# Kernel optimization log

Hardware: AMD Instinct MI355X
Metric: run time of the kernel (lower is better)

## Reference

```python
import jax, jax.numpy as jnp
import numpy as np

NUM_HEAD = 8
HIDDEN = 128
INPUT_DIM = 256
N1 = 1024
N2 = 1024
BATCH = 16


def setup_inputs() -> dict:
    key = jax.random.key(0)
    ks = jax.random.split(key, 10)
    HD = HIDDEN * NUM_HEAD  # 1024
    return {
        "x1": jax.random.normal(ks[0], (BATCH, N1, INPUT_DIM), jnp.float32),
        "x2": jax.random.normal(ks[1], (BATCH, N2, INPUT_DIM), jnp.float32),
        "B": jax.random.normal(ks[2], (N1, N2), jnp.float32),
        "wq_w": jax.random.normal(ks[3], (HD, INPUT_DIM), jnp.float32) * 0.02,
        "wq_b": jnp.zeros((HD,), jnp.float32),
        "wk_w": jax.random.normal(ks[4], (HD, INPUT_DIM), jnp.float32) * 0.02,
        "wk_b": jnp.zeros((HD,), jnp.float32),
        "wv_w": jax.random.normal(ks[5], (HD, INPUT_DIM), jnp.float32) * 0.02,
        "wv_b": jnp.zeros((HD,), jnp.float32),
        "proj_w": jax.random.normal(ks[6], (HIDDEN, HD), jnp.float32) * 0.02,
        "proj_b": jnp.zeros((HIDDEN,), jnp.float32),
    }


def reference(x1, x2, B, wq_w, wq_b, wk_w, wk_b, wv_w, wv_b, proj_w, proj_b):
    b, n1, _ = x1.shape
    n2 = x2.shape[1]
    sdk = jnp.sqrt(jnp.asarray(HIDDEN, x1.dtype))
    # Linear layers (torch convention: y = x @ W.T + b)
    q = x1 @ wq_w.T + wq_b                      # [b, n1, H*D]
    k = x2 @ wk_w.T + wk_b                      # [b, n2, H*D]
    v = x2 @ wv_w.T + wv_b                      # [b, n2, H*D]
    q = q.reshape(b, n1, NUM_HEAD, HIDDEN)
    k = k.reshape(b, n2, NUM_HEAD, HIDDEN)
    v = v.reshape(b, n2, NUM_HEAD, HIDDEN)
    # scores: [b, h, n1, n2]
    scores = jnp.einsum("bnhd,bmhd->bhnm", q, k) / sdk + B[None, None, :, :]
    attn = jax.nn.softmax(scores, axis=-1)
    out = jnp.einsum("bhnm,bmhd->bnhd", attn, v).reshape(b, n1, NUM_HEAD * HIDDEN)
    return out @ proj_w.T + proj_b              # [b, n1, HIDDEN]
```

## Files before the change

### kernel.cpp

```cpp
#include <hip/hip_runtime.h>
#include <hip/hip_fp16.h>

typedef _Float16 f16;
typedef __attribute__((ext_vector_type(4))) _Float16 f16x4;
typedef __attribute__((ext_vector_type(8))) _Float16 f16x8;
typedef __attribute__((ext_vector_type(4))) float f32x4;

#define MFMA_F16(a,b,c) __builtin_amdgcn_mfma_f32_16x16x32_f16((a),(b),(c),0,0,0)

__device__ __forceinline__ void gl_lds16(const f16* g, f16* l) {
  __builtin_amdgcn_global_load_lds(
      (const __attribute__((address_space(1))) unsigned int*)g,
      (__attribute__((address_space(3))) unsigned int*)l, 16, 0, 0);
}


__global__ __launch_bounds__(256) void gemm_qkv(
    const float* __restrict__ x1, const float* __restrict__ x2,
    const float* __restrict__ wq, const float* __restrict__ wqb,
    const float* __restrict__ wk, const float* __restrict__ wkb,
    const float* __restrict__ wv, const float* __restrict__ wvb,
    f16* __restrict__ Qp, f16* __restrict__ Kp, f16* __restrict__ Vp,
    float qscale) {
  constexpr int LD = 72;
  __shared__ f16 As[128][LD];
  __shared__ f16 Bs[128][LD];
  const int z = blockIdx.z;
  const float* X    = (z == 0) ? x1 : x2;
  const float* W    = (z == 0) ? wq : (z == 1) ? wk : wv;
  const float* bias = (z == 0) ? wqb : (z == 1) ? wkb : wvb;
  f16* outp         = (z == 0) ? Qp : (z == 1) ? Kp : Vp;
  const float sc    = (z == 0) ? qscale : 1.0f;

  const int tid = threadIdx.x, lane = tid & 63, wid = tid >> 6;
  const int col = lane & 15, quad = lane >> 4;
  const int wm = (wid >> 1) * 64, wn = (wid & 1) * 64;
  const int n0x = blockIdx.x * 128;
  const int m0w = blockIdx.y * 128;

  f32x4 acc[4][4];
#pragma unroll
  for (int i = 0; i < 4; i++)
#pragma unroll
    for (int j = 0; j < 4; j++) acc[i][j] = (f32x4){0.f, 0.f, 0.f, 0.f};

  for (int kt = 0; kt < 4; ++kt) {
    const int k0 = kt * 64;
#pragma unroll
    for (int i = 0; i < 8; i++) {
      int f = i * 256 + tid;
      int r = f >> 4, c4 = f & 15;
      float4 v = *(const float4*)(W + (size_t)(m0w + r) * 256 + k0 + c4 * 4);
      f16x4 hh; hh[0] = (f16)v.x; hh[1] = (f16)v.y; hh[2] = (f16)v.z; hh[3] = (f16)v.w;
      *(f16x4*)&As[r][c4 * 4] = hh;
    }
#pragma unroll
    for (int i = 0; i < 8; i++) {
      int f = i * 256 + tid;
      int r = f >> 4, c4 = f & 15;
      float4 v = *(const float4*)(X + (size_t)(n0x + r) * 256 + k0 + c4 * 4);
      f16x4 hh; hh[0] = (f16)v.x; hh[1] = (f16)v.y; hh[2] = (f16)v.z; hh[3] = (f16)v.w;
      *(f16x4*)&Bs[r][c4 * 4] = hh;
    }
    __syncthreads();
    const f16 (*Rs)[LD] = (z == 2) ? Bs : As;
    const f16 (*Cs)[LD] = (z == 2) ? As : Bs;
#pragma unroll
    for (int ks = 0; ks < 2; ks++) {
      f16x8 af[4], bf[4];
#pragma unroll
      for (int i = 0; i < 4; i++) af[i] = *(const f16x8*)&Rs[wm + i * 16 + col][ks * 32 + quad * 8];
#pragma unroll
      for (int j = 0; j < 4; j++) bf[j] = *(const f16x8*)&Cs[wn + j * 16 + col][ks * 32 + quad * 8];
#pragma unroll
      for (int i = 0; i < 4; i++)
#pragma unroll
        for (int j = 0; j < 4; j++) acc[i][j] = MFMA_F16(af[i], bf[j], acc[i][j]);
    }
    __syncthreads();
  }

  const int h = blockIdx.y;
  if (z < 2) {
#pragma unroll
    for (int i = 0; i < 4; i++) {
      const int k0h = wm + i * 16 + quad * 4;
      float4 bq = *(const float4*)(bias + h * 128 + k0h);
      const int ks2 = k0h >> 5, q2 = (k0h >> 3) & 3, lo = k0h & 7;
#pragma unroll
      for (int j = 0; j < 4; j++) {
        const int bn2 = n0x + wn + j * 16 + col;
        const int b = bn2 >> 10, n2 = bn2 & 1023;
        const int T = n2 >> 6, jt = (n2 >> 4) & 3, c2 = n2 & 15;
        f16x4 pk;
#pragma unroll
        for (int r = 0; r < 4; r++)
          pk[r] = (f16)((acc[i][j][r] + ((const float*)&bq)[r]) * sc);
        *(f16x4*)(outp + (size_t)(b * 8 + h) * 131072 + T * 8192 +
                  (jt * 4 + ks2) * 512 + (q2 * 16 + c2) * 8 + lo) = pk;
      }
    }
  } else {
#pragma unroll
    for (int j = 0; j < 4; j++) {
      const int d = wn + j * 16 + col;
      const float bv = bias[h * 128 + d];
      const int ct = d >> 4, c2 = d & 15;
#pragma unroll
      for (int i = 0; i < 4; i++) {
        const int bn2 = n0x + wm + i * 16 + quad * 4;
        const int b = bn2 >> 10, n2 = bn2 & 1023;
        const int T = n2 >> 6, kv0 = n2 & 63;
        const int ks2 = kv0 >> 5, q2 = (kv0 >> 3) & 3, lo = kv0 & 7;
        f16x4 pk;
#pragma unroll
        for (int r = 0; r < 4; r++) pk[r] = (f16)(acc[i][j][r] + bv);
        *(f16x4*)(outp + (size_t)(b * 8 + h) * 131072 + T * 8192 +
                  (ct * 2 + ks2) * 512 + (q2 * 16 + c2) * 8 + lo) = pk;
      }
    }
  }
}

__global__ __launch_bounds__(256) void gemm_proj(const f16* __restrict__ A,
                                                 const float* __restrict__ W,
                                                 const float* __restrict__ bias,
                                                 float* __restrict__ out) {
  constexpr int LD = 72;
  __shared__ f16 As[64][LD];
  __shared__ f16 Bs[64][LD];
  const int tid = threadIdx.x, lane = tid & 63, wid = tid >> 6;
  const int col = lane & 15, quad = lane >> 4;
  const int wm = (wid >> 1) * 32, wn = (wid & 1) * 32;
  const int m0 = blockIdx.x * 64, n0 = blockIdx.y * 64;

  f32x4 acc[2][2];
#pragma unroll
  for (int i = 0; i < 2; i++)
#pragma unroll
    for (int j = 0; j < 2; j++) acc[i][j] = (f32x4){0.f, 0.f, 0.f, 0.f};

  for (int kt = 0; kt < 16; ++kt) {
    const int k0 = kt * 64;
#pragma unroll
    for (int i = 0; i < 2; i++) {
      int f = i * 256 + tid;
      int r = f >> 3, ch = f & 7;
      *(f16x8*)&As[r][ch * 8] = *(const f16x8*)(A + (size_t)(m0 + r) * 1024 + k0 + ch * 8);
    }
#pragma unroll
    for (int i = 0; i < 4; i++) {
      int f = i * 256 + tid;
      int r = f >> 4, c4 = f & 15;
      float4 v = *(const float4*)(W + (size_t)(n0 + r) * 1024 + k0 + c4 * 4);
      f16x4 hh; hh[0] = (f16)v.x; hh[1] = (f16)v.y; hh[2] = (f16)v.z; hh[3] = (f16)v.w;
      *(f16x4*)&Bs[r][c4 * 4] = hh;
    }
    __syncthreads();
#pragma unroll
    for (int ks = 0; ks < 2; ks++) {
      f16x8 af[2], bf[2];
#pragma unroll
      for (int i = 0; i < 2; i++) af[i] = *(const f16x8*)&As[wm + i * 16 + col][ks * 32 + quad * 8];
#pragma unroll
      for (int j = 0; j < 2; j++) bf[j] = *(const f16x8*)&Bs[wn + j * 16 + col][ks * 32 + quad * 8];
#pragma unroll
      for (int i = 0; i < 2; i++)
#pragma unroll
        for (int j = 0; j < 2; j++) acc[i][j] = MFMA_F16(af[i], bf[j], acc[i][j]);
    }
    __syncthreads();
  }
#pragma unroll
  for (int j = 0; j < 2; j++) {
    const int c = n0 + wn + j * 16 + col;
    const float bv = bias[c];
#pragma unroll
    for (int i = 0; i < 2; i++) {
      const int r0 = m0 + wm + i * 16 + quad * 4;
#pragma unroll
      for (int r = 0; r < 4; r++)
        out[(size_t)(r0 + r) * 128 + c] = acc[i][j][r] + bv;
    }
  }
}

__global__ __launch_bounds__(256) __attribute__((amdgpu_waves_per_eu(2, 2)))
void attn_fused(const f16* __restrict__ Qp, const f16* __restrict__ Kp,
                const f16* __restrict__ Vp, const float* __restrict__ Bm,
                f16* __restrict__ O) {
  __shared__ f16 Ksl[2][8192];
  __shared__ f16 Vtl[2][8192];
  __shared__ f16 Ps[8192];
  const int tid = threadIdx.x, lane = tid & 63, wid = tid >> 6;
  const int col = lane & 15, quad = lane >> 4;
  const int id = blockIdx.x;
  const int mt = (id >> 3) & 7;
  const int bh = ((id >> 6) << 3) | (id & 7);
  const int b = bh >> 3, h = bh & 7;
  const int m0 = mt * 128;
  const int wm = wid * 32;

  const f16* Qb = Qp + (size_t)bh * 131072;
  const f16* Kb = Kp + (size_t)bh * 131072;
  const f16* Vb = Vp + (size_t)bh * 131072;

#define ISSUE(T, bufi)                                                       \
  {                                                                          \
    _Pragma("unroll") for (int j = 0; j < 4; j++) {                          \
      gl_lds16(Kb + (size_t)(T) * 8192 + (wid * 4 + j) * 512 + lane * 8,     \
               &Ksl[bufi][(wid * 4 + j) * 512]);                             \
      gl_lds16(Vb + (size_t)(T) * 8192 + (wid * 4 + j) * 512 + lane * 8,     \
               &Vtl[bufi][(wid * 4 + j) * 512]);                             \
    }                                                                        \
  }

  ISSUE(0, 0);
  ISSUE(1, 1);

  f16x8 qf[2][4];
#pragma unroll
  for (int i = 0; i < 2; i++) {
    const int m = m0 + wm + i * 16;
#pragma unroll
    for (int ks = 0; ks < 4; ks++)
      qf[i][ks] = *(const f16x8*)(Qb + (m >> 6) * 8192 +
                                  (((m >> 4) & 3) * 4 + ks) * 512 + lane * 8);
  }

  f32x4 oacc[2][8];
  float l[2] = {0.f, 0.f};
#pragma unroll
  for (int i = 0; i < 2; i++)
#pragma unroll
    for (int ct = 0; ct < 8; ct++) oacc[i][ct] = (f32x4){0.f, 0.f, 0.f, 0.f};

  __syncthreads();

  for (int t = 0; t < 16; ++t) {
    const int buf = t & 1;
    const int n0 = t * 64;

    float4 breg[2][4];
#pragma unroll
    for (int i = 0; i < 2; i++) {
      const float* Brow = Bm + (size_t)(m0 + wm + i * 16 + col) * 1024 + n0;
#pragma unroll
      for (int jt = 0; jt < 4; jt++)
        breg[i][jt] = *(const float4*)(Brow + jt * 16 + quad * 4);
    }

    f32x4 s[2][4];
#pragma unroll
    for (int i = 0; i < 2; i++)
#pragma unroll
      for (int jt = 0; jt < 4; jt++) s[i][jt] = (f32x4){0.f, 0.f, 0.f, 0.f};
#pragma unroll
    for (int ks = 0; ks < 4; ks++) {
      f16x8 kf[4];
#pragma unroll
      for (int jt = 0; jt < 4; jt++)
        kf[jt] = *(const f16x8*)&Ksl[buf][(jt * 4 + ks) * 512 + lane * 8];
#pragma unroll
      for (int i = 0; i < 2; i++)
#pragma unroll
        for (int jt = 0; jt < 4; jt++) s[i][jt] = MFMA_F16(kf[jt], qf[i][ks], s[i][jt]);
    }

#pragma unroll
    for (int i = 0; i < 2; i++) {
      const int m = wm + i * 16 + col;
#pragma unroll
      for (int jt = 0; jt < 4; jt++) {
        const float* bv = (const float*)&breg[i][jt];
        float p0 = __expf(s[i][jt][0] + bv[0]);
        float p1 = __expf(s[i][jt][1] + bv[1]);
        float p2 = __expf(s[i][jt][2] + bv[2]);
        float p3 = __expf(s[i][jt][3] + bv[3]);
        l[i] += (p0 + p1) + (p2 + p3);
        f16x4 pk; pk[0] = (f16)p0; pk[1] = (f16)p1; pk[2] = (f16)p2; pk[3] = (f16)p3;
        const int g = (jt * 2 + (quad >> 1)) ^ (col & 7);
        *(f16x4*)&Ps[m * 64 + g * 8 + (quad & 1) * 4] = pk;
      }
    }

#pragma unroll
    for (int ks = 0; ks < 2; ks++) {
      f16x8 pf[2];
#pragma unroll
      for (int i = 0; i < 2; i++) {
        const int m = wm + i * 16 + col;
        const int g = (ks * 4 + quad) ^ (col & 7);
        pf[i] = *(const f16x8*)&Ps[m * 64 + g * 8];
      }
      f16x8 vf[8];
#pragma unroll
      for (int ct = 0; ct < 8; ct++)
        vf[ct] = *(const f16x8*)&Vtl[buf][(ct * 2 + ks) * 512 + lane * 8];
#pragma unroll
      for (int i = 0; i < 2; i++)
#pragma unroll
        for (int ct = 0; ct < 8; ct++)
          oacc[i][ct] = MFMA_F16(pf[i], vf[ct], oacc[i][ct]);
    }

    __syncthreads();
    if (t + 2 < 16) ISSUE(t + 2, buf);
  }

#pragma unroll
  for (int i = 0; i < 2; i++) {
    l[i] += __shfl_xor(l[i], 16);
    l[i] += __shfl_xor(l[i], 32);
  }
  f16* Ob = O + ((size_t)(b * 1024 + m0 + wm)) * 1024 + h * 128;
#pragma unroll
  for (int i = 0; i < 2; i++)
#pragma unroll
    for (int r = 0; r < 4; r++) {
      const float lv = __shfl(l[i], (lane & 48) | (quad * 4 + r));
      const float inv = 1.0f / lv;
#pragma unroll
      for (int ct = 0; ct < 8; ct++)
        Ob[(size_t)(i * 16 + quad * 4 + r) * 1024 + ct * 16 + col] =
            (f16)(oacc[i][ct][r] * inv);
    }
}

extern "C" void kernel_launch(void* const* d_in, const int* in_sizes, int n_in,
                              void* d_out, int out_size, void* d_ws, size_t ws_size,
                              hipStream_t stream) {
  (void)in_sizes; (void)n_in; (void)out_size; (void)ws_size;
  const float* x1  = (const float*)d_in[0];
  const float* x2  = (const float*)d_in[1];
  const float* Bm  = (const float*)d_in[2];
  const float* wq  = (const float*)d_in[3];
  const float* wqb = (const float*)d_in[4];
  const float* wk  = (const float*)d_in[5];
  const float* wkb = (const float*)d_in[6];
  const float* wv  = (const float*)d_in[7];
  const float* wvb = (const float*)d_in[8];
  const float* pw  = (const float*)d_in[9];
  const float* pb  = (const float*)d_in[10];
  float* out = (float*)d_out;

  const size_t ELEMS = (size_t)16 * 1024 * 1024;
  f16* Qp = (f16*)d_ws;
  f16* Kp = Qp + ELEMS;
  f16* Vp = Kp + ELEMS;
  f16* Ow = Vp + ELEMS;

  const float scale = 0.0883883476483184f;
  dim3 blk(256);
  gemm_qkv<<<dim3(128, 8, 3), blk, 0, stream>>>(x1, x2, wq, wqb, wk, wkb, wv, wvb,
                                                Qp, Kp, Vp, scale);
  attn_fused<<<dim3(1024), blk, 0, stream>>>(Qp, Kp, Vp, Bm, Ow);
  gemm_proj<<<dim3(256, 2), blk, 0, stream>>>(Ow, pw, pb, out);
}
```

Baseline: 288.1 us.

## Split attention work across eight waves and register-prefetch QKV GEMM tiles

The attention kernel now runs 512 threads per block, with each wave handling 16 query rows instead of 32. K and V loads are split so four waves fetch K and four fetch V. This halves per-wave accumulator state and aims for higher occupancy and latency hiding, at the cost of less reuse of each K/V fragment read from LDS. The QKV projection GEMM also prefetches the next k-tile from global memory into registers while the current tile is computed, overlapping load latency with MFMA work at the cost of extra registers.

Result: no change. 284.6 us (-1.2%).

```diff
diff --git a/kernel.cpp b/kernel.cpp
--- a/kernel.cpp
+++ b/kernel.cpp
@@ -38,31 +38,40 @@
   const int n0x = blockIdx.x * 128;
   const int m0w = blockIdx.y * 128;
 
+  const int rr = tid >> 4, cc4 = tid & 15;
+
   f32x4 acc[4][4];
 #pragma unroll
   for (int i = 0; i < 4; i++)
 #pragma unroll
     for (int j = 0; j < 4; j++) acc[i][j] = (f32x4){0.f, 0.f, 0.f, 0.f};
 
+  float4 wreg[8], xreg[8];
+#pragma unroll
+  for (int i = 0; i < 8; i++) {
+    wreg[i] = *(const float4*)(W + (size_t)(m0w + rr + i * 16) * 256 + cc4 * 4);
+    xreg[i] = *(const float4*)(X + (size_t)(n0x + rr + i * 16) * 256 + cc4 * 4);
+  }
+
   for (int kt = 0; kt < 4; ++kt) {
-    const int k0 = kt * 64;
 #pragma unroll
     for (int i = 0; i < 8; i++) {
-      int f = i * 256 + tid;
-      int r = f >> 4, c4 = f & 15;
-      float4 v = *(const float4*)(W + (size_t)(m0w + r) * 256 + k0 + c4 * 4);
+      float4 v = wreg[i];
       f16x4 hh; hh[0] = (f16)v.x; hh[1] = (f16)v.y; hh[2] = (f16)v.z; hh[3] = (f16)v.w;
-      *(f16x4*)&As[r][c4 * 4] = hh;
-    }
-#pragma unroll
-    for (int i = 0; i < 8; i++) {
-      int f = i * 256 + tid;
-      int r = f >> 4, c4 = f & 15;
-      float4 v = *(const float4*)(X + (size_t)(n0x + r) * 256 + k0 + c4 * 4);
-      f16x4 hh; hh[0] = (f16)v.x; hh[1] = (f16)v.y; hh[2] = (f16)v.z; hh[3] = (f16)v.w;
-      *(f16x4*)&Bs[r][c4 * 4] = hh;
-    }
-    __syncthreads();
+      *(f16x4*)&As[rr + i * 16][cc4 * 4] = hh;
+      v = xreg[i];
+      f16x4 hg; hg[0] = (f16)v.x; hg[1] = (f16)v.y; hg[2] = (f16)v.z; hg[3] = (f16)v.w;
+      *(f16x4*)&Bs[rr + i * 16][cc4 * 4] = hg;
+    }
+    __syncthreads();
+    if (kt < 3) {
+      const int k0 = (kt + 1) * 64;
+#pragma unroll
+      for (int i = 0; i < 8; i++) {
+        wreg[i] = *(const float4*)(W + (size_t)(m0w + rr + i * 16) * 256 + k0 + cc4 * 4);
+        xreg[i] = *(const float4*)(X + (size_t)(n0x + rr + i * 16) * 256 + k0 + cc4 * 4);
+      }
+    }
     const f16 (*Rs)[LD] = (z == 2) ? Bs : As;
     const f16 (*Cs)[LD] = (z == 2) ? As : Bs;
 #pragma unroll
@@ -185,7 +194,7 @@
   }
 }
 
-__global__ __launch_bounds__(256) __attribute__((amdgpu_waves_per_eu(2, 2)))
+__global__ __launch_bounds__(512) __attribute__((amdgpu_waves_per_eu(4, 4)))
 void attn_fused(const f16* __restrict__ Qp, const f16* __restrict__ Kp,
                 const f16* __restrict__ Vp, const float* __restrict__ Bm,
                 f16* __restrict__ O) {
@@ -199,41 +208,41 @@
   const int bh = ((id >> 6) << 3) | (id & 7);
   const int b = bh >> 3, h = bh & 7;
   const int m0 = mt * 128;
-  const int wm = wid * 32;
+  const int wm = wid * 16;
 
   const f16* Qb = Qp + (size_t)bh * 131072;
   const f16* Kb = Kp + (size_t)bh * 131072;
   const f16* Vb = Vp + (size_t)bh * 131072;
 
-#define ISSUE(T, bufi)                                                       \
-  {                                                                          \
-    _Pragma("unroll") for (int j = 0; j < 4; j++) {                          \
-      gl_lds16(Kb + (size_t)(T) * 8192 + (wid * 4 + j) * 512 + lane * 8,     \
-               &Ksl[bufi][(wid * 4 + j) * 512]);                             \
-      gl_lds16(Vb + (size_t)(T) * 8192 + (wid * 4 + j) * 512 + lane * 8,     \
-               &Vtl[bufi][(wid * 4 + j) * 512]);                             \
-    }                                                                        \
+#define ISSUE(T, bufi)                                                        \
+  {                                                                           \
+    if (wid < 4) {                                                            \
+      _Pragma("unroll") for (int j = 0; j < 4; j++)                           \
+          gl_lds16(Kb + (size_t)(T) * 8192 + (wid * 4 + j) * 512 + lane * 8,  \
+                   &Ksl[bufi][(wid * 4 + j) * 512]);                          \
+    } else {                                                                  \
+      _Pragma("unroll") for (int j = 0; j < 4; j++)                           \
+          gl_lds16(Vb + (size_t)(T) * 8192 + ((wid - 4) * 4 + j) * 512 + lane * 8, \
+                   &Vtl[bufi][((wid - 4) * 4 + j) * 512]);                    \
+    }                                                                         \
   }
 
   ISSUE(0, 0);
   ISSUE(1, 1);
 
-  f16x8 qf[2][4];
-#pragma unroll
-  for (int i = 0; i < 2; i++) {
-    const int m = m0 + wm + i * 16;
+  f16x8 qf[4];
+  {
+    const int m = m0 + wm;
+    const int T = m >> 6, jt2 = (m >> 4) & 3;
 #pragma unroll
     for (int ks = 0; ks < 4; ks++)
-      qf[i][ks] = *(const f16x8*)(Qb + (m >> 6) * 8192 +
-                                  (((m >> 4) & 3) * 4 + ks) * 512 + lane * 8);
-  }
-
-  f32x4 oacc[2][8];
-  float l[2] = {0.f, 0.f};
-#pragma unroll
-  for (int i = 0; i < 2; i++)
-#pragma unroll
-    for (int ct = 0; ct < 8; ct++) oacc[i][ct] = (f32x4){0.f, 0.f, 0.f, 0.f};
+      qf[ks] = *(const f16x8*)(Qb + T * 8192 + (jt2 * 4 + ks) * 512 + lane * 8);
+  }
+
+  f32x4 oacc[8];
+  float l = 0.f;
+#pragma unroll
+  for (int ct = 0; ct < 8; ct++) oacc[ct] = (f32x4){0.f, 0.f, 0.f, 0.f};
 
   __syncthreads();
 
@@ -241,20 +250,17 @@
     const int buf = t & 1;
     const int n0 = t * 64;
 
-    float4 breg[2][4];
-#pragma unroll
-    for (int i = 0; i < 2; i++) {
-      const float* Brow = Bm + (size_t)(m0 + wm + i * 16 + col) * 1024 + n0;
+    float4 breg[4];
+    {
+      const float* Brow = Bm + (size_t)(m0 + wm + col) * 1024 + n0;
 #pragma unroll
       for (int jt = 0; jt < 4; jt++)
-        breg[i][jt] = *(const float4*)(Brow + jt * 16 + quad * 4);
-    }
-
-    f32x4 s[2][4];
-#pragma unroll
-    for (int i = 0; i < 2; i++)
-#pragma unroll
-      for (int jt = 0; jt < 4; jt++) s[i][jt] = (f32x4){0.f, 0.f, 0.f, 0.f};
+        breg[jt] = *(const float4*)(Brow + jt * 16 + quad * 4);
+    }
+
+    f32x4 s[4];
+#pragma unroll
+    for (int jt = 0; jt < 4; jt++) s[jt] = (f32x4){0.f, 0.f, 0.f, 0.f};
 #pragma unroll
     for (int ks = 0; ks < 4; ks++) {
       f16x8 kf[4];
@@ -262,22 +268,19 @@
       for (int jt = 0; jt < 4; jt++)
         kf[jt] = *(const f16x8*)&Ksl[buf][(jt * 4 + ks) * 512 + lane * 8];
 #pragma unroll
-      for (int i = 0; i < 2; i++)
-#pragma unroll
-        for (int jt = 0; jt < 4; jt++) s[i][jt] = MFMA_F16(kf[jt], qf[i][ks], s[i][jt]);
-    }
-
-#pragma unroll
-    for (int i = 0; i < 2; i++) {
-      const int m = wm + i * 16 + col;
+      for (int jt = 0; jt < 4; jt++) s[jt] = MFMA_F16(kf[jt], qf[ks], s[jt]);
+    }
+
+    {
+      const int m = wm + col;
 #pragma unroll
       for (int jt = 0; jt < 4; jt++) {
-        const float* bv = (const float*)&breg[i][jt];
-        float p0 = __expf(s[i][jt][0] + bv[0]);
-        float p1 = __expf(s[i][jt][1] + bv[1]);
-        float p2 = __expf(s[i][jt][2] + bv[2]);
-        float p3 = __expf(s[i][jt][3] + bv[3]);
-        l[i] += (p0 + p1) + (p2 + p3);
+        const float* bv = (const float*)&breg[jt];
+        float p0 = __expf(s[jt][0] + bv[0]);
+        float p1 = __expf(s[jt][1] + bv[1]);
+        float p2 = __expf(s[jt][2] + bv[2]);
+        float p3 = __expf(s[jt][3] + bv[3]);
+        l += (p0 + p1) + (p2 + p3);
         f16x4 pk; pk[0] = (f16)p0; pk[1] = (f16)p1; pk[2] = (f16)p2; pk[3] = (f16)p3;
         const int g = (jt * 2 + (quad >> 1)) ^ (col & 7);
         *(f16x4*)&Ps[m * 64 + g * 8 + (quad & 1) * 4] = pk;
@@ -286,45 +289,31 @@
 
 #pragma unroll
     for (int ks = 0; ks < 2; ks++) {
-      f16x8 pf[2];
-#pragma unroll
-      for (int i = 0; i < 2; i++) {
-        const int m = wm + i * 16 + col;
-        const int g = (ks * 4 + quad) ^ (col & 7);
-        pf[i] = *(const f16x8*)&Ps[m * 64 + g * 8];
-      }
-      f16x8 vf[8];
-#pragma unroll
-      for (int ct = 0; ct < 8; ct++)
-        vf[ct] = *(const f16x8*)&Vtl[buf][(ct * 2 + ks) * 512 + lane * 8];
-#pragma unroll
-      for (int i = 0; i < 2; i++)
-#pragma unroll
-        for (int ct = 0; ct < 8; ct++)
-          oacc[i][ct] = MFMA_F16(pf[i], vf[ct], oacc[i][ct]);
+      const int m = wm + col;
+      const int g = (ks * 4 + quad) ^ (col & 7);
+      f16x8 pf = *(const f16x8*)&Ps[m * 64 + g * 8];
+#pragma unroll
+      for (int ct = 0; ct < 8; ct++) {
+        f16x8 vf = *(const f16x8*)&Vtl[buf][(ct * 2 + ks) * 512 + lane * 8];
+        oacc[ct] = MFMA_F16(pf, vf, oacc[ct]);
+      }
     }
 
     __syncthreads();
     if (t + 2 < 16) ISSUE(t + 2, buf);
   }
 
-#pragma unroll
-  for (int i = 0; i < 2; i++) {
-    l[i] += __shfl_xor(l[i], 16);
-    l[i] += __shfl_xor(l[i], 32);
-  }
+  l += __shfl_xor(l, 16);
+  l += __shfl_xor(l, 32);
   f16* Ob = O + ((size_t)(b * 1024 + m0 + wm)) * 1024 + h * 128;
 #pragma unroll
-  for (int i = 0; i < 2; i++)
-#pragma unroll
-    for (int r = 0; r < 4; r++) {
-      const float lv = __shfl(l[i], (lane & 48) | (quad * 4 + r));
-      const float inv = 1.0f / lv;
-#pragma unroll
-      for (int ct = 0; ct < 8; ct++)
-        Ob[(size_t)(i * 16 + quad * 4 + r) * 1024 + ct * 16 + col] =
-            (f16)(oacc[i][ct][r] * inv);
-    }
+  for (int r = 0; r < 4; r++) {
+    const float lv = __shfl(l, (lane & 48) | (quad * 4 + r));
+    const float inv = 1.0f / lv;
+#pragma unroll
+    for (int ct = 0; ct < 8; ct++)
+      Ob[(size_t)(quad * 4 + r) * 1024 + ct * 16 + col] = (f16)(oacc[ct][r] * inv);
+  }
 }
 
 extern "C" void kernel_launch(void* const* d_in, const int* in_sizes, int n_in,
@@ -351,9 +340,8 @@
   f16* Ow = Vp + ELEMS;
 
   const float scale = 0.0883883476483184f;
-  dim3 blk(256);
-  gemm_qkv<<<dim3(128, 8, 3), blk, 0, stream>>>(x1, x2, wq, wqb, wk, wkb, wv, wvb,
-                                                Qp, Kp, Vp, scale);
-  attn_fused<<<dim3(1024), blk, 0, stream>>>(Qp, Kp, Vp, Bm, Ow);
-  gemm_proj<<<dim3(256, 2), blk, 0, stream>>>(Ow, pw, pb, out);
-}
+  gemm_qkv<<<dim3(128, 8, 3), dim3(256), 0, stream>>>(x1, x2, wq, wqb, wk, wkb,
+                                                      wv, wvb, Qp, Kp, Vp, scale);
+  attn_fused<<<dim3(1024), dim3(512), 0, stream>>>(Qp, Kp, Vp, Bm, Ow);
+  gemm_proj<<<dim3(256, 2), dim3(256), 0, stream>>>(Ow, pw, pb, out);
+}
```
